# Optimization experiments

Hardware: AMD Instinct MI355X
Metric: run time of the kernel (lower is better)

Reference implementation:

```python
import math
import jax, jax.numpy as jnp
import numpy as np


def setup_inputs() -> dict:
    key = jax.random.key(0)
    T, C = 8192, 2048
    layer_depth, num_layers = 5, 10
    ks = jax.random.split(key, 8)

    x = jax.random.normal(ks[0], (T, C), jnp.float32)
    sx = jax.random.normal(ks[1], (C,), jnp.float32)
    aa = jnp.zeros((C,), jnp.float32)
    bb = jnp.zeros((C,), jnp.float32)
    pp = jnp.zeros((C,), jnp.float32)

    # parameter initial values per TimeMix.setup
    r01 = layer_depth / (num_layers - 1)
    r10 = 1.0 - layer_depth / num_layers
    zigzag = 0.5 * (jnp.arange(1, C + 1) % 3 - 1).astype(jnp.float32)
    time_first = jnp.full((C,), math.log(0.3), jnp.float32) + zigzag
    h = jnp.arange(C, dtype=jnp.float32)
    time_decay = (-5.0 + 8.0 * (h / (C - 1)) ** (0.7 + 1.3 * r01)).astype(jnp.float32)
    xr = jnp.arange(C, dtype=jnp.float32) / C
    time_mix_k = xr ** r10
    time_mix_v = time_mix_k + 0.3 * r01
    time_mix_r = xr ** (0.5 * r10)

    ln_scale = jnp.ones((C,), jnp.float32)
    ln_bias = jnp.zeros((C,), jnp.float32)

    s = 1.0 / np.sqrt(C)  # lecun-normal-ish scale for Dense kernels
    Wk = jax.random.normal(ks[2], (C, C), jnp.float32) * s
    Wv = jax.random.normal(ks[3], (C, C), jnp.float32) * s
    Wr = jax.random.normal(ks[4], (C, C), jnp.float32) * s
    Wo = jax.random.normal(ks[5], (C, C), jnp.float32) * s

    return dict(x=x, sx=sx, aa=aa, bb=bb, pp=pp,
                time_first=time_first, time_decay=time_decay,
                time_mix_k=time_mix_k, time_mix_v=time_mix_v, time_mix_r=time_mix_r,
                ln_scale=ln_scale, ln_bias=ln_bias,
                Wk=Wk, Wv=Wv, Wr=Wr, Wo=Wo)


def reference(x, sx, aa, bb, pp, time_first, time_decay,
              time_mix_k, time_mix_v, time_mix_r,
              ln_scale, ln_bias, Wk, Wv, Wr, Wo):
    # LayerNorm(eps=1e-5)
    mu = jnp.mean(x, axis=-1, keepdims=True)
    var = jnp.var(x, axis=-1, keepdims=True)
    xx = (x - mu) * jax.lax.rsqrt(var + 1e-5) * ln_scale + ln_bias  # [T, C]

    # token shift: previous timestep (sx state for t=0)
    sxs = jnp.concatenate((sx[None, :], xx[:-1, :]), axis=0)  # [T, C]
    kx = xx * time_mix_k + sxs * (1.0 - time_mix_k)
    vx = xx * time_mix_v + sxs * (1.0 - time_mix_v)
    rx = xx * time_mix_r + sxs * (1.0 - time_mix_r)

    r = jax.nn.sigmoid(rx @ Wr)  # [T, C]
    k = kx @ Wk                  # [T, C]
    v = vx @ Wv                  # [T, C]

    w = -jnp.exp(time_decay)     # [C]

    def step(state, kv):
        aa, bb, pp = state
        kk, vv = kv
        # output with numerically-stable log-sum-exp style bookkeeping
        ww = time_first + kk
        p = jnp.maximum(pp, ww)
        e1 = jnp.exp(pp - p)
        e2 = jnp.exp(ww - p)
        out = ((e1 * aa + e2 * vv) / (e1 * bb + e2)).astype(r.dtype)
        # state update
        ww2 = w + pp
        p2 = jnp.maximum(ww2, kk)
        e1b = jnp.exp(ww2 - p2)
        e2b = jnp.exp(kk - p2)
        aa = e1b * aa + e2b * vv
        bb = e1b * bb + e2b
        return (aa, bb, p2), out

    (aa, bb, pp), wkv = jax.lax.scan(step, (aa, bb, pp), (k, v))  # wkv: [T, C]

    out = x + (r * wkv) @ Wo
    return (out, xx[-1, :], aa, bb, pp)
```

## Files before the change

### kernel.cpp

```cpp
#include <hip/hip_runtime.h>
#include <stdint.h>

#define T_DIM 8192
#define C_DIM 2048
#define LCHUNK 32
#define NCHUNK (T_DIM / LCHUNK)

typedef unsigned short u16;
typedef __bf16 bf16x8_t __attribute__((ext_vector_type(8)));
typedef float f32x4_t __attribute__((ext_vector_type(4)));

__device__ __forceinline__ u16 f2bf(float f) {
    union { float f; uint32_t u; } x; x.f = f;
    uint32_t r = x.u + 0x7fffu + ((x.u >> 16) & 1u);
    return (u16)(r >> 16);
}
__device__ __forceinline__ float bf2f(u16 u) {
    union { uint32_t u; float f; } x; x.u = ((uint32_t)u) << 16;
    return x.f;
}
__device__ __forceinline__ void gload16(const void* g, void* l) {
    __builtin_amdgcn_global_load_lds((const __attribute__((address_space(1))) uint32_t*)g,
                                     (__attribute__((address_space(3))) uint32_t*)l, 16, 0, 0);
}
__device__ __forceinline__ f32x4_t mfma16(bf16x8_t a, bf16x8_t b, f32x4_t c) {
    return __builtin_amdgcn_mfma_f32_16x16x32_bf16(a, b, c, 0, 0, 0);
}

__device__ __forceinline__ void transpose_tile(const float* __restrict__ W, u16* __restrict__ Tm,
                                               int bn, int bk, float* shf)
{
    const int tid = threadIdx.x;
    const int tx = tid & 31, ty = tid >> 5;
#pragma unroll
    for (int i = 0; i < 4; ++i)
        shf[(ty + 8 * i) * 33 + tx] = W[(size_t)(bk + ty + 8 * i) * C_DIM + bn + tx];
    __syncthreads();
#pragma unroll
    for (int i = 0; i < 4; ++i)
        Tm[(size_t)(bn + ty + 8 * i) * C_DIM + bk + tx] = f2bf(shf[tx * 33 + ty + 8 * i]);
}

union F8 { float4 v[2]; float f[8]; };

__global__ __launch_bounds__(256)
void prep_kernel(const float* __restrict__ W0, const float* __restrict__ W1,
                 const float* __restrict__ W2, u16* __restrict__ Wt,
                 const float* __restrict__ x, const float* __restrict__ sx,
                 const float* __restrict__ lns, const float* __restrict__ lnb,
                 const float* __restrict__ tmk, const float* __restrict__ tmv,
                 const float* __restrict__ tmr,
                 u16* __restrict__ kx, u16* __restrict__ vx, u16* __restrict__ rx,
                 float* __restrict__ xx_last)
{
    __shared__ float shf[32 * 33];
    const int bid = blockIdx.x;
    const int tid = threadIdx.x;

    if (bid >= 8192) {
        const int z = (bid - 8192) >> 12;
        const int rem = (bid - 8192) & 4095;
        const float* W = (z == 0) ? W0 : (z == 1) ? W1 : W2;
        transpose_tile(W, Wt + (size_t)z * C_DIM * C_DIM, (rem & 63) * 32, (rem >> 6) * 32, shf);
        return;
    }

    const int t = bid;
    const size_t rowoff = (size_t)t * C_DIM;

    F8 a, p;
    const float4* xt = (const float4*)(x + rowoff);
    a.v[0] = xt[2 * tid]; a.v[1] = xt[2 * tid + 1];
    const float4* xp = (t == 0) ? (const float4*)sx : (const float4*)(x + rowoff - C_DIM);
    p.v[0] = xp[2 * tid]; p.v[1] = xp[2 * tid + 1];

    float s1 = 0.f, s2 = 0.f, s3 = 0.f, s4 = 0.f;
#pragma unroll
    for (int i = 0; i < 8; ++i) {
        s1 += a.f[i]; s2 += a.f[i] * a.f[i];
        s3 += p.f[i]; s4 += p.f[i] * p.f[i];
    }
#pragma unroll
    for (int off = 32; off; off >>= 1) {
        s1 += __shfl_down(s1, off);
        s2 += __shfl_down(s2, off);
        s3 += __shfl_down(s3, off);
        s4 += __shfl_down(s4, off);
    }
    float* red = shf;
    if ((tid & 63) == 0) {
        red[0 * 4 + (tid >> 6)] = s1; red[1 * 4 + (tid >> 6)] = s2;
        red[2 * 4 + (tid >> 6)] = s3; red[3 * 4 + (tid >> 6)] = s4;
    }
    __syncthreads();
    s1 = red[0] + red[1] + red[2] + red[3];
    s2 = red[4] + red[5] + red[6] + red[7];
    s3 = red[8] + red[9] + red[10] + red[11];
    s4 = red[12] + red[13] + red[14] + red[15];
    const float inv = 1.0f / (float)C_DIM;
    const float mu = s1 * inv;
    const float rstd = rsqrtf(s2 * inv - mu * mu + 1e-5f);
    const float mup = s3 * inv;
    const float rstdp = rsqrtf(s4 * inv - mup * mup + 1e-5f);

    F8 ls, lb, mk, mv, mr;
    { const float4* q = (const float4*)lns; ls.v[0] = q[2*tid]; ls.v[1] = q[2*tid+1]; }
    { const float4* q = (const float4*)lnb; lb.v[0] = q[2*tid]; lb.v[1] = q[2*tid+1]; }
    { const float4* q = (const float4*)tmk; mk.v[0] = q[2*tid]; mk.v[1] = q[2*tid+1]; }
    { const float4* q = (const float4*)tmv; mv.v[0] = q[2*tid]; mv.v[1] = q[2*tid+1]; }
    { const float4* q = (const float4*)tmr; mr.v[0] = q[2*tid]; mr.v[1] = q[2*tid+1]; }

    union { u16 u[8]; uint4 q; } ok, ov, orr;
#pragma unroll
    for (int i = 0; i < 8; ++i) {
        const float xxv  = (a.f[i] - mu) * rstd * ls.f[i] + lb.f[i];
        const float prev = (t == 0) ? p.f[i] : (p.f[i] - mup) * rstdp * ls.f[i] + lb.f[i];
        ok.u[i]  = f2bf(xxv * mk.f[i] + prev * (1.f - mk.f[i]));
        ov.u[i]  = f2bf(xxv * mv.f[i] + prev * (1.f - mv.f[i]));
        orr.u[i] = f2bf(xxv * mr.f[i] + prev * (1.f - mr.f[i]));
        if (t == T_DIM - 1) xx_last[tid * 8 + i] = xxv;
    }
    ((uint4*)(kx + rowoff))[tid] = ok.q;
    ((uint4*)(vx + rowoff))[tid] = ov.q;
    ((uint4*)(rx + rowoff))[tid] = orr.q;
}

__device__ __forceinline__ void gemm_core_db(
    const u16* __restrict__ A, const u16* __restrict__ Bt,
    void* __restrict__ Cout, const float* __restrict__ resid,
    const int mode, const int N, const int K, const int m0, const int n0, u16* lds)
{
    const int tid = threadIdx.x;
    const int wave = tid >> 6, lane = tid & 63;
    const int wm = wave >> 1, wn = wave & 1;
    const int fr = lane & 15, fo = lane >> 4;
    const int sw = (fo ^ ((fr >> 1) & 3)) * 8;

    f32x4_t acc[4][4] = {};

    const int lrow = lane >> 2;
    const int scol = ((lane & 3) ^ ((lane >> 3) & 3)) * 8;
    const u16* gA = A  + (size_t)(m0 + wave * 16 + lrow) * K + scol;
    const u16* gB = Bt + (size_t)(n0 + wave * 16 + lrow) * K + scol;
    const size_t rk64 = (size_t)64 * K;
    const int dA = wave * 512;
    const int dB = 4096 + wave * 512;

    auto stage = [&](int t) {
        const int b = (t & 1) * 8192;
        const u16* ga = gA + (size_t)t * 32;
        const u16* gb = gB + (size_t)t * 32;
        gload16(ga,        lds + b + dA);
        gload16(ga + rk64, lds + b + dA + 2048);
        gload16(gb,        lds + b + dB);
        gload16(gb + rk64, lds + b + dB + 2048);
    };

    const int NT = K >> 5;
    stage(0);
    asm volatile("s_waitcnt vmcnt(0)" ::: "memory");
    asm volatile("s_barrier" ::: "memory");

    for (int t = 0; t < NT; ++t) {
        if (t + 1 < NT) stage(t + 1);
        const u16* lA = lds + (t & 1) * 8192 + (wm * 64 + fr) * 32;
        const u16* lB = lds + (t & 1) * 8192 + 4096 + (wn * 64 + fr) * 32;
        bf16x8_t a[4], b[4];
#pragma unroll
        for (int i = 0; i < 4; ++i) {
            a[i] = *(const bf16x8_t*)(lA + i * 512 + sw);
            b[i] = *(const bf16x8_t*)(lB + i * 512 + sw);
        }
        __builtin_amdgcn_s_setprio(1);
#pragma unroll
        for (int mi = 0; mi < 4; ++mi)
#pragma unroll
            for (int ni = 0; ni < 4; ++ni)
                acc[mi][ni] = mfma16(a[mi], b[ni], acc[mi][ni]);
        __builtin_amdgcn_s_setprio(0);
        asm volatile("s_waitcnt vmcnt(0)" ::: "memory");
        asm volatile("s_barrier" ::: "memory");
    }

    const int r4 = fo * 4;
#pragma unroll
    for (int mi = 0; mi < 4; ++mi) {
#pragma unroll
        for (int ni = 0; ni < 4; ++ni) {
            const int col = n0 + wn * 64 + ni * 16 + fr;
#pragma unroll
            for (int i = 0; i < 4; ++i) {
                const int row = m0 + wm * 64 + mi * 16 + r4 + i;
                float v = acc[mi][ni][i];
                if (mode == 0) {
                    ((float*)Cout)[(size_t)row * N + col] = v + resid[(size_t)row * N + col];
                } else if (mode == 1) {
                    ((u16*)Cout)[(size_t)row * N + col] = f2bf(v);
                } else {
                    const float s = 1.f / (1.f + __expf(-v));
                    ((u16*)Cout)[(size_t)row * N + col] = f2bf(s);
                }
            }
        }
    }
}

__global__ __launch_bounds__(256, 4)
void gemm_kvr(const u16* __restrict__ kx, const u16* __restrict__ vx, const u16* __restrict__ rxp,
              const float* __restrict__ Wo, u16* __restrict__ Wt,
              u16* __restrict__ kbuf, u16* __restrict__ vbuf, u16* __restrict__ rbuf)
{
    __shared__ u16 lds[16384];
    const int bid = blockIdx.x;
    if (bid >= 3072) {
        const int rem = bid - 3072;
        transpose_tile(Wo, Wt + (size_t)3 * C_DIM * C_DIM, (rem & 63) * 32, (rem >> 6) * 32,
                       (float*)lds);
        return;
    }
    const int which = bid >> 10;
    const int b = bid & 1023;
    const int m0 = (b & 63) << 7;
    const int n0 = (b >> 6) << 7;
    const u16* A = (which == 0) ? kx : (which == 1) ? vx : rxp;
    const u16* B = Wt + (size_t)which * C_DIM * C_DIM;
    u16* C = (which == 0) ? kbuf : (which == 1) ? vbuf : rbuf;
    gemm_core_db(A, B, C, nullptr, (which == 2) ? 2 : 1, C_DIM, C_DIM, m0, n0, lds);
}

__global__ __launch_bounds__(256, 4)
void gemm_o(const u16* __restrict__ Aw, const u16* __restrict__ Wt3,
            float* __restrict__ out, const float* __restrict__ x)
{
    __shared__ u16 lds[16384];
    const int m0 = (int)(blockIdx.x & 63) << 7;
    const int n0 = (int)(blockIdx.x >> 6) << 7;
    gemm_core_db(Aw, Wt3, out, x, 0, C_DIM, C_DIM, m0, n0, lds);
}

__global__ __launch_bounds__(256)
void scan_partial(const u16* __restrict__ k, const u16* __restrict__ v,
                  const float* __restrict__ time_decay,
                  float* __restrict__ pA, float* __restrict__ pB, float* __restrict__ pP)
{
    const int j = blockIdx.x;
    const int c0 = threadIdx.x * 8;
    float w8[8];
    {
        F8 t; const float4* q = (const float4*)(time_decay + c0);
        t.v[0] = q[0]; t.v[1] = q[1];
#pragma unroll
        for (int i = 0; i < 8; ++i) w8[i] = -__expf(t.f[i]);
    }
    float aa[8] = {}, bb[8] = {}, pp[8];
#pragma unroll
    for (int i = 0; i < 8; ++i) pp[i] = -1e30f;

    const u16* kp = k + (size_t)j * LCHUNK * C_DIM + c0;
    const u16* vp = v + (size_t)j * LCHUNK * C_DIM + c0;
    for (int s = 0; s < LCHUNK; ++s) {
        union { uint4 q; u16 u[8]; } kq, vq;
        kq.q = *(const uint4*)kp; vq.q = *(const uint4*)vp;
        kp += C_DIM; vp += C_DIM;
#pragma unroll
        for (int i = 0; i < 8; ++i) {
            const float kk = bf2f(kq.u[i]);
            const float vv = bf2f(vq.u[i]);
            const float ww = w8[i] + pp[i];
            const float p2 = fmaxf(ww, kk);
            const float e1 = __expf(ww - p2);
            const float e2 = __expf(kk - p2);
            aa[i] = e1 * aa[i] + e2 * vv;
            bb[i] = e1 * bb[i] + e2;
            pp[i] = p2;
        }
    }
    const int o = j * C_DIM + c0;
    *(float4*)(pA + o)     = make_float4(aa[0], aa[1], aa[2], aa[3]);
    *(float4*)(pA + o + 4) = make_float4(aa[4], aa[5], aa[6], aa[7]);
    *(float4*)(pB + o)     = make_float4(bb[0], bb[1], bb[2], bb[3]);
    *(float4*)(pB + o + 4) = make_float4(bb[4], bb[5], bb[6], bb[7]);
    *(float4*)(pP + o)     = make_float4(pp[0], pp[1], pp[2], pp[3]);
    *(float4*)(pP + o + 4) = make_float4(pp[4], pp[5], pp[6], pp[7]);
}

__global__ __launch_bounds__(256)
void scan_combine(const float* __restrict__ pA, const float* __restrict__ pB,
                  const float* __restrict__ pP,
                  const float* __restrict__ aa_in, const float* __restrict__ bb_in,
                  const float* __restrict__ pp_in,
                  const float* __restrict__ time_decay,
                  float* __restrict__ sA, float* __restrict__ sB, float* __restrict__ sP)
{
    const int c = blockIdx.x * 256 + threadIdx.x;
    const float wL = -__expf(time_decay[c]) * (float)LCHUNK;
    float a = aa_in[c], b = bb_in[c], p = pp_in[c];
    float Ab[8], Bb[8], Pb[8];
#pragma unroll
    for (int i = 0; i < 8; ++i) {
        const int o = i * C_DIM + c;
        Ab[i] = pA[o]; Bb[i] = pB[o]; Pb[i] = pP[o];
    }
    for (int j0 = 0; j0 < NCHUNK; j0 += 8) {
        float An[8], Bn[8], Pn[8];
        if (j0 + 8 < NCHUNK) {
#pragma unroll
            for (int i = 0; i < 8; ++i) {
                const int o = (j0 + 8 + i) * C_DIM + c;
                An[i] = pA[o]; Bn[i] = pB[o]; Pn[i] = pP[o];
            }
        } else {
#pragma unroll
            for (int i = 0; i < 8; ++i) { An[i] = 0.f; Bn[i] = 0.f; Pn[i] = 0.f; }
        }
#pragma unroll
        for (int i = 0; i < 8; ++i) {
            const int o = (j0 + i) * C_DIM + c;
            sA[o] = a; sB[o] = b; sP[o] = p;
            const float pd = p + wL;
            const float q = fmaxf(pd, Pb[i]);
            const float e1 = __expf(pd - q), e2 = __expf(Pb[i] - q);
            a = e1 * a + e2 * Ab[i];
            b = e1 * b + e2 * Bb[i];
            p = q;
        }
#pragma unroll
        for (int i = 0; i < 8; ++i) { Ab[i] = An[i]; Bb[i] = Bn[i]; Pb[i] = Pn[i]; }
    }
}

__global__ __launch_bounds__(256)
void scan_out(const u16* __restrict__ k, const u16* __restrict__ v,
              const u16* __restrict__ r,
              const float* __restrict__ time_decay, const float* __restrict__ time_first,
              const float* __restrict__ sA, const float* __restrict__ sB,
              const float* __restrict__ sP,
              u16* __restrict__ arwkv,
              float* __restrict__ aa_out, float* __restrict__ bb_out, float* __restrict__ pp_out)
{
    const int j = blockIdx.x;
    const int c0 = threadIdx.x * 8;
    float w8[8], u8[8];
    {
        F8 t; const float4* q = (const float4*)(time_decay + c0);
        t.v[0] = q[0]; t.v[1] = q[1];
#pragma unroll
        for (int i = 0; i < 8; ++i) w8[i] = -__expf(t.f[i]);
        const float4* q2 = (const float4*)(time_first + c0);
        t.v[0] = q2[0]; t.v[1] = q2[1];
#pragma unroll
        for (int i = 0; i < 8; ++i) u8[i] = t.f[i];
    }
    float aa[8], bb[8], pp[8];
    {
        const int so = j * C_DIM + c0;
        F8 t;
        t.v[0] = ((const float4*)(sA + so))[0]; t.v[1] = ((const float4*)(sA + so))[1];
#pragma unroll
        for (int i = 0; i < 8; ++i) aa[i] = t.f[i];
        t.v[0] = ((const float4*)(sB + so))[0]; t.v[1] = ((const float4*)(sB + so))[1];
#pragma unroll
        for (int i = 0; i < 8; ++i) bb[i] = t.f[i];
        t.v[0] = ((const float4*)(sP + so))[0]; t.v[1] = ((const float4*)(sP + so))[1];
#pragma unroll
        for (int i = 0; i < 8; ++i) pp[i] = t.f[i];
    }

    const size_t base = (size_t)j * LCHUNK * C_DIM + c0;
    const u16* kp = k + base;
    const u16* vp = v + base;
    const u16* rp = r + base;
    u16* op = arwkv + base;
    for (int s = 0; s < LCHUNK; ++s) {
        union { uint4 q; u16 u[8]; } kq, vq, rq, oq;
        kq.q = *(const uint4*)kp; vq.q = *(const uint4*)vp; rq.q = *(const uint4*)rp;
        kp += C_DIM; vp += C_DIM; rp += C_DIM;
#pragma unroll
        for (int i = 0; i < 8; ++i) {
            const float kk = bf2f(kq.u[i]);
            const float vv = bf2f(vq.u[i]);
            const float sr = bf2f(rq.u[i]);
            const float ww = u8[i] + kk;
            const float p = fmaxf(pp[i], ww);
            const float e1 = __expf(pp[i] - p);
            const float e2 = __expf(ww - p);
            const float o = (e1 * aa[i] + e2 * vv) / (e1 * bb[i] + e2);
            oq.u[i] = f2bf(sr * o);
            const float ww2 = w8[i] + pp[i];
            const float p2 = fmaxf(ww2, kk);
            const float f1 = __expf(ww2 - p2);
            const float f2 = __expf(kk - p2);
            aa[i] = f1 * aa[i] + f2 * vv;
            bb[i] = f1 * bb[i] + f2;
            pp[i] = p2;
        }
        *(uint4*)op = oq.q;
        op += C_DIM;
    }
    if (j == NCHUNK - 1) {
#pragma unroll
        for (int i = 0; i < 8; ++i) {
            aa_out[c0 + i] = aa[i]; bb_out[c0 + i] = bb[i]; pp_out[c0 + i] = pp[i];
        }
    }
}

extern "C" void kernel_launch(void* const* d_in, const int* in_sizes, int n_in,
                              void* d_out, int out_size, void* d_ws, size_t ws_size,
                              hipStream_t stream)
{
    (void)in_sizes; (void)n_in; (void)out_size; (void)ws_size;
    const float* x          = (const float*)d_in[0];
    const float* sx         = (const float*)d_in[1];
    const float* aa_in      = (const float*)d_in[2];
    const float* bb_in      = (const float*)d_in[3];
    const float* pp_in      = (const float*)d_in[4];
    const float* time_first = (const float*)d_in[5];
    const float* time_decay = (const float*)d_in[6];
    const float* tmk        = (const float*)d_in[7];
    const float* tmv        = (const float*)d_in[8];
    const float* tmr        = (const float*)d_in[9];
    const float* lns        = (const float*)d_in[10];
    const float* lnb        = (const float*)d_in[11];
    const float* Wk         = (const float*)d_in[12];
    const float* Wv         = (const float*)d_in[13];
    const float* Wr         = (const float*)d_in[14];
    const float* Wo         = (const float*)d_in[15];

    float* out     = (float*)d_out;
    float* xx_last = out + (size_t)T_DIM * C_DIM;
    float* aa_out  = xx_last + C_DIM;
    float* bb_out  = aa_out + C_DIM;
    float* pp_out  = bb_out + C_DIM;

    const size_t TC = (size_t)T_DIM * C_DIM;
    const size_t C2 = (size_t)C_DIM * C_DIM;
    u16* kx    = (u16*)d_ws;
    u16* vx    = kx + TC;
    u16* rx    = vx + TC;
    u16* Wt    = rx + TC;
    u16* kbuf  = Wt + 4 * C2;
    u16* vbuf  = kbuf + TC;
    u16* rbuf  = vbuf + TC;
    float* pA  = (float*)(rbuf + TC);
    float* pB  = pA + (size_t)NCHUNK * C_DIM;
    float* pP  = pB + (size_t)NCHUNK * C_DIM;
    float* sA  = pP + (size_t)NCHUNK * C_DIM;
    float* sB  = sA + (size_t)NCHUNK * C_DIM;
    float* sP  = sB + (size_t)NCHUNK * C_DIM;
    u16* arwkv = rx;

    prep_kernel<<<8192 + 12288, 256, 0, stream>>>(Wk, Wv, Wr, Wt,
                                                  x, sx, lns, lnb, tmk, tmv, tmr,
                                                  kx, vx, rx, xx_last);
    gemm_kvr<<<3072 + 4096, 256, 0, stream>>>(kx, vx, rx, Wo, Wt, kbuf, vbuf, rbuf);
    scan_partial<<<NCHUNK, 256, 0, stream>>>(kbuf, vbuf, time_decay, pA, pB, pP);
    scan_combine<<<C_DIM / 256, 256, 0, stream>>>(pA, pB, pP, aa_in, bb_in, pp_in, time_decay, sA, sB, sP);
    scan_out<<<NCHUNK, 256, 0, stream>>>(kbuf, vbuf, rbuf, time_decay, time_first,
                                         sA, sB, sP, arwkv, aa_out, bb_out, pp_out);
    gemm_o<<<1024, 256, 0, stream>>>(arwkv, Wt + 3 * C2, out, x);
}
```

Baseline: 475.7 us.

## Split scan kernels across channel blocks and double chunk length

New measurement: 463.6 us. 2.5% less time.

```diff
diff --git a/kernel.cpp b/kernel.cpp
--- a/kernel.cpp
+++ b/kernel.cpp
@@ -3,7 +3,7 @@
 
 #define T_DIM 8192
 #define C_DIM 2048
-#define LCHUNK 32
+#define LCHUNK 64
 #define NCHUNK (T_DIM / LCHUNK)
 
 typedef unsigned short u16;
@@ -244,44 +244,37 @@
                   float* __restrict__ pA, float* __restrict__ pB, float* __restrict__ pP)
 {
     const int j = blockIdx.x;
-    const int c0 = threadIdx.x * 8;
-    float w8[8];
-    {
-        F8 t; const float4* q = (const float4*)(time_decay + c0);
-        t.v[0] = q[0]; t.v[1] = q[1];
-#pragma unroll
-        for (int i = 0; i < 8; ++i) w8[i] = -__expf(t.f[i]);
-    }
-    float aa[8] = {}, bb[8] = {}, pp[8];
-#pragma unroll
-    for (int i = 0; i < 8; ++i) pp[i] = -1e30f;
+    const int c0 = blockIdx.y * 512 + threadIdx.x * 2;
+    const float2 td = *(const float2*)(time_decay + c0);
+    const float w0 = -__expf(td.x), w1 = -__expf(td.y);
+    float aa0 = 0.f, bb0 = 0.f, pp0 = -1e30f;
+    float aa1 = 0.f, bb1 = 0.f, pp1 = -1e30f;
 
     const u16* kp = k + (size_t)j * LCHUNK * C_DIM + c0;
     const u16* vp = v + (size_t)j * LCHUNK * C_DIM + c0;
     for (int s = 0; s < LCHUNK; ++s) {
-        union { uint4 q; u16 u[8]; } kq, vq;
-        kq.q = *(const uint4*)kp; vq.q = *(const uint4*)vp;
+        const uint32_t kq = *(const uint32_t*)kp;
+        const uint32_t vq = *(const uint32_t*)vp;
         kp += C_DIM; vp += C_DIM;
-#pragma unroll
-        for (int i = 0; i < 8; ++i) {
-            const float kk = bf2f(kq.u[i]);
-            const float vv = bf2f(vq.u[i]);
-            const float ww = w8[i] + pp[i];
+        {
+            const float kk = bf2f((u16)kq), vv = bf2f((u16)vq);
+            const float ww = w0 + pp0;
             const float p2 = fmaxf(ww, kk);
-            const float e1 = __expf(ww - p2);
-            const float e2 = __expf(kk - p2);
-            aa[i] = e1 * aa[i] + e2 * vv;
-            bb[i] = e1 * bb[i] + e2;
-            pp[i] = p2;
+            const float e1 = __expf(ww - p2), e2 = __expf(kk - p2);
+            aa0 = e1 * aa0 + e2 * vv; bb0 = e1 * bb0 + e2; pp0 = p2;
+        }
+        {
+            const float kk = bf2f((u16)(kq >> 16)), vv = bf2f((u16)(vq >> 16));
+            const float ww = w1 + pp1;
+            const float p2 = fmaxf(ww, kk);
+            const float e1 = __expf(ww - p2), e2 = __expf(kk - p2);
+            aa1 = e1 * aa1 + e2 * vv; bb1 = e1 * bb1 + e2; pp1 = p2;
         }
     }
     const int o = j * C_DIM + c0;
-    *(float4*)(pA + o)     = make_float4(aa[0], aa[1], aa[2], aa[3]);
-    *(float4*)(pA + o + 4) = make_float4(aa[4], aa[5], aa[6], aa[7]);
-    *(float4*)(pB + o)     = make_float4(bb[0], bb[1], bb[2], bb[3]);
-    *(float4*)(pB + o + 4) = make_float4(bb[4], bb[5], bb[6], bb[7]);
-    *(float4*)(pP + o)     = make_float4(pp[0], pp[1], pp[2], pp[3]);
-    *(float4*)(pP + o + 4) = make_float4(pp[4], pp[5], pp[6], pp[7]);
+    *(float2*)(pA + o) = make_float2(aa0, aa1);
+    *(float2*)(pB + o) = make_float2(bb0, bb1);
+    *(float2*)(pP + o) = make_float2(pp0, pp1);
 }
 
 __global__ __launch_bounds__(256)
@@ -339,32 +332,17 @@
               float* __restrict__ aa_out, float* __restrict__ bb_out, float* __restrict__ pp_out)
 {
     const int j = blockIdx.x;
-    const int c0 = threadIdx.x * 8;
-    float w8[8], u8[8];
-    {
-        F8 t; const float4* q = (const float4*)(time_decay + c0);
-        t.v[0] = q[0]; t.v[1] = q[1];
-#pragma unroll
-        for (int i = 0; i < 8; ++i) w8[i] = -__expf(t.f[i]);
-        const float4* q2 = (const float4*)(time_first + c0);
-        t.v[0] = q2[0]; t.v[1] = q2[1];
-#pragma unroll
-        for (int i = 0; i < 8; ++i) u8[i] = t.f[i];
-    }
-    float aa[8], bb[8], pp[8];
-    {
-        const int so = j * C_DIM + c0;
-        F8 t;
-        t.v[0] = ((const float4*)(sA + so))[0]; t.v[1] = ((const float4*)(sA + so))[1];
-#pragma unroll
-        for (int i = 0; i < 8; ++i) aa[i] = t.f[i];
-        t.v[0] = ((const float4*)(sB + so))[0]; t.v[1] = ((const float4*)(sB + so))[1];
-#pragma unroll
-        for (int i = 0; i < 8; ++i) bb[i] = t.f[i];
-        t.v[0] = ((const float4*)(sP + so))[0]; t.v[1] = ((const float4*)(sP + so))[1];
-#pragma unroll
-        for (int i = 0; i < 8; ++i) pp[i] = t.f[i];
-    }
+    const int c0 = blockIdx.y * 512 + threadIdx.x * 2;
+    const float2 td = *(const float2*)(time_decay + c0);
+    const float2 tf = *(const float2*)(time_first + c0);
+    const float w0 = -__expf(td.x), w1 = -__expf(td.y);
+    const float u0 = tf.x, u1 = tf.y;
+
+    const int so = j * C_DIM + c0;
+    float2 a2 = *(const float2*)(sA + so);
+    float2 b2 = *(const float2*)(sB + so);
+    float2 p2v = *(const float2*)(sP + so);
+    float aa0 = a2.x, aa1 = a2.y, bb0 = b2.x, bb1 = b2.y, pp0 = p2v.x, pp1 = p2v.y;
 
     const size_t base = (size_t)j * LCHUNK * C_DIM + c0;
     const u16* kp = k + base;
@@ -372,36 +350,42 @@
     const u16* rp = r + base;
     u16* op = arwkv + base;
     for (int s = 0; s < LCHUNK; ++s) {
-        union { uint4 q; u16 u[8]; } kq, vq, rq, oq;
-        kq.q = *(const uint4*)kp; vq.q = *(const uint4*)vp; rq.q = *(const uint4*)rp;
+        const uint32_t kq = *(const uint32_t*)kp;
+        const uint32_t vq = *(const uint32_t*)vp;
+        const uint32_t rq = *(const uint32_t*)rp;
         kp += C_DIM; vp += C_DIM; rp += C_DIM;
-#pragma unroll
-        for (int i = 0; i < 8; ++i) {
-            const float kk = bf2f(kq.u[i]);
-            const float vv = bf2f(vq.u[i]);
-            const float sr = bf2f(rq.u[i]);
-            const float ww = u8[i] + kk;
-            const float p = fmaxf(pp[i], ww);
-            const float e1 = __expf(pp[i] - p);
-            const float e2 = __expf(ww - p);
-            const float o = (e1 * aa[i] + e2 * vv) / (e1 * bb[i] + e2);
-            oq.u[i] = f2bf(sr * o);
-            const float ww2 = w8[i] + pp[i];
-            const float p2 = fmaxf(ww2, kk);
-            const float f1 = __expf(ww2 - p2);
-            const float f2 = __expf(kk - p2);
-            aa[i] = f1 * aa[i] + f2 * vv;
-            bb[i] = f1 * bb[i] + f2;
-            pp[i] = p2;
-        }
-        *(uint4*)op = oq.q;
+        uint32_t oq;
+        {
+            const float kk = bf2f((u16)kq), vv = bf2f((u16)vq), sr = bf2f((u16)rq);
+            const float ww = u0 + kk;
+            const float p = fmaxf(pp0, ww);
+            const float e1 = __expf(pp0 - p), e2 = __expf(ww - p);
+            const float o = (e1 * aa0 + e2 * vv) / (e1 * bb0 + e2);
+            oq = (uint32_t)f2bf(sr * o);
+            const float ww2 = w0 + pp0;
+            const float q = fmaxf(ww2, kk);
+            const float f1 = __expf(ww2 - q), f2v = __expf(kk - q);
+            aa0 = f1 * aa0 + f2v * vv; bb0 = f1 * bb0 + f2v; pp0 = q;
+        }
+        {
+            const float kk = bf2f((u16)(kq >> 16)), vv = bf2f((u16)(vq >> 16)), sr = bf2f((u16)(rq >> 16));
+            const float ww = u1 + kk;
+            const float p = fmaxf(pp1, ww);
+            const float e1 = __expf(pp1 - p), e2 = __expf(ww - p);
+            const float o = (e1 * aa1 + e2 * vv) / (e1 * bb1 + e2);
+            oq |= ((uint32_t)f2bf(sr * o)) << 16;
+            const float ww2 = w1 + pp1;
+            const float q = fmaxf(ww2, kk);
+            const float f1 = __expf(ww2 - q), f2v = __expf(kk - q);
+            aa1 = f1 * aa1 + f2v * vv; bb1 = f1 * bb1 + f2v; pp1 = q;
+        }
+        *(uint32_t*)op = oq;
         op += C_DIM;
     }
     if (j == NCHUNK - 1) {
-#pragma unroll
-        for (int i = 0; i < 8; ++i) {
-            aa_out[c0 + i] = aa[i]; bb_out[c0 + i] = bb[i]; pp_out[c0 + i] = pp[i];
-        }
+        aa_out[c0] = aa0; aa_out[c0 + 1] = aa1;
+        bb_out[c0] = bb0; bb_out[c0 + 1] = bb1;
+        pp_out[c0] = pp0; pp_out[c0 + 1] = pp1;
     }
 }
 
@@ -454,9 +438,9 @@
                                                   x, sx, lns, lnb, tmk, tmv, tmr,
                                                   kx, vx, rx, xx_last);
     gemm_kvr<<<3072 + 4096, 256, 0, stream>>>(kx, vx, rx, Wo, Wt, kbuf, vbuf, rbuf);
-    scan_partial<<<NCHUNK, 256, 0, stream>>>(kbuf, vbuf, time_decay, pA, pB, pP);
+    scan_partial<<<dim3(NCHUNK, 4), 256, 0, stream>>>(kbuf, vbuf, time_decay, pA, pB, pP);
     scan_combine<<<C_DIM / 256, 256, 0, stream>>>(pA, pB, pP, aa_in, bb_in, pp_in, time_decay, sA, sB, sP);
-    scan_out<<<NCHUNK, 256, 0, stream>>>(kbuf, vbuf, rbuf, time_decay, time_first,
-                                         sA, sB, sP, arwkv, aa_out, bb_out, pp_out);
+    scan_out<<<dim3(NCHUNK, 4), 256, 0, stream>>>(kbuf, vbuf, rbuf, time_decay, time_first,
+                                                  sA, sB, sP, arwkv, aa_out, bb_out, pp_out);
     gemm_o<<<1024, 256, 0, stream>>>(arwkv, Wt + 3 * C2, out, x);
 }
```
